# Optimization experiments

Hardware: AMD Instinct MI355X
Metric: run time of the kernel (lower is better)

The kernel has to match this reference:

```python
import jax, jax.numpy as jnp
import numpy as np

N = 10000   # nodes
E = 320000  # edges
B = 4       # batch
D = 128     # in_dim == out_dim
H = 4       # heads
DH = D // H # 32, per-head dim
OUT_L = D // H  # per-layer out_fc output dim (out_dim/num_heads)
NEG_SLOPE = 0.1


def setup_inputs() -> dict:
    key = jax.random.key(0)
    ks = jax.random.split(key, 20)
    inp = {
        "features": jax.random.normal(ks[0], (B, N, D), dtype=jnp.float32),
        "src": jax.random.randint(ks[1], (E,), 0, N),
        "dst": jax.random.randint(ks[2], (E,), 0, N),
        "edge_w": jax.random.uniform(ks[3], (E,), dtype=jnp.float32),
    }
    s = 0.05
    for l in range(2):
        k = 4 + 5 * l
        inp[f"fc_w{l}"] = jax.random.normal(ks[k], (D, D), dtype=jnp.float32) * s
        inp[f"al{l}"] = jax.random.normal(ks[k + 1], (H, DH), dtype=jnp.float32) * s
        inp[f"ar{l}"] = jax.random.normal(ks[k + 2], (H, DH), dtype=jnp.float32) * s
        inp[f"out_w{l}"] = jax.random.normal(ks[k + 3], (OUT_L, DH), dtype=jnp.float32) * s
        inp[f"out_b{l}"] = jnp.zeros((OUT_L,), dtype=jnp.float32)
    inp["mlp_w"] = jax.random.normal(ks[14], (D, 2 * D), dtype=jnp.float32) * s
    inp["mlp_b"] = jnp.zeros((D,), dtype=jnp.float32)
    return inp


def _gat_layer(x, src, dst, w, fc_w, al, ar, out_w, out_b):
    # x: [B,N,D]
    feat = jnp.einsum("bnd,ed->bne", x, fc_w).reshape(B, N, H, DH)  # fc, no bias
    el = jnp.einsum("bnhd,hd->bnh", feat, al)  # [B,N,H]
    er = jnp.einsum("bnhd,hd->bnh", feat, ar)
    # per-edge scores, edge-major: [E,B,H]
    e = jnp.moveaxis(el[:, src] + er[:, dst], 1, 0)
    e = jnp.where(e > 0, e, NEG_SLOPE * e)        # LeakyReLU(0.1)
    e = e * w[:, None, None]                      # edge weight applied pre-softmax
    # edge-softmax over incoming edges of each dst node
    m = jax.ops.segment_max(e, dst, num_segments=N)
    m = jnp.where(jnp.isfinite(m), m, 0.0)
    ex = jnp.exp(e - m[dst])
    den = jax.ops.segment_sum(ex, dst, num_segments=N)[dst]
    a = ex / jnp.where(den == 0, 1.0, den)        # [E,B,H]
    # u_mul_e + sum aggregation
    feat_n = jnp.moveaxis(feat, 0, 1)             # [N,B,H,DH]
    msg = feat_n[src] * a[..., None]              # [E,B,H,DH]
    agg = jax.ops.segment_sum(msg, dst, num_segments=N)  # [N,B,H,DH]
    out = jax.nn.relu(jnp.einsum("nbhd,od->nbho", agg, out_w) + out_b)
    # transpose(0,1) then concat heads along feature dim -> [B,N,H*OUT_L]
    return jnp.moveaxis(out, 0, 1).reshape(B, N, H * OUT_L)


def reference(features, src, dst, edge_w,
              fc_w0, al0, ar0, out_w0, out_b0,
              fc_w1, al1, ar1, out_w1, out_b1,
              mlp_w, mlp_b):
    x1 = _gat_layer(features, src, dst, edge_w, fc_w0, al0, ar0, out_w0, out_b0)
    x2 = _gat_layer(x1, src, dst, edge_w, fc_w1, al1, ar1, out_w1, out_b1)
    h = jnp.concatenate([x1, x2], axis=-1)        # [B,N,2*D]
    return jnp.einsum("bnk,ok->bno", h, mlp_w) + mlp_b  # eval mode: dropout off
```

## Files before the change

kernel.cpp:

```cpp
#include <hip/hip_runtime.h>
#include <hip/hip_fp16.h>
#include <float.h>

#define NN 10000
#define EE 320000
#define BB 4
#define DD 128
#define HH 4
#define DHH 32

union H4 { uint2 u2; __half2 h2[2]; };
union H8 { float4 f4; __half2 h2[4]; };

typedef _Float16 f16x8 __attribute__((ext_vector_type(8)));
typedef float f32x4 __attribute__((ext_vector_type(4)));

__global__ void pack_weights(const float* __restrict__ fc0, const float* __restrict__ fc1,
                             const float* __restrict__ mlp,
                             __half* __restrict__ bp0, __half* __restrict__ bp1,
                             __half* __restrict__ bpm,
                             int* __restrict__ cnt, int* __restrict__ cursor) {
    int s = blockIdx.x * 256 + threadIdx.x;
    int i = s & 7, l = (s >> 3) & 63, ct = (s >> 9) & 7, kt = s >> 12;
    int k = kt * 32 + 8 * (l >> 4) + i;
    int o = ct * 16 + (l & 15);
    bpm[s] = __float2half(mlp[o * 256 + k]);
    if (s < 16384) {
        bp0[s] = __float2half(fc0[o * 128 + k]);
        bp1[s] = __float2half(fc1[o * 128 + k]);
    }
    if (s < NN) { cnt[s] = 0; cursor[s] = 0; }
}

__global__ void count_edges(const int* __restrict__ dst, int* __restrict__ cnt) {
    int e = blockIdx.x * 256 + threadIdx.x;
    if (e < EE) atomicAdd(&cnt[dst[e]], 1);
}

__global__ void scan_kernel(const int* __restrict__ cnt, int* __restrict__ row_off) {
    __shared__ int part[1024];
    int t = threadIdx.x;
    const int CH = 10;
    int loc[CH];
    int s = 0;
#pragma unroll
    for (int j = 0; j < CH; ++j) {
        int i = t * CH + j;
        int v = (i < NN) ? cnt[i] : 0;
        loc[j] = s;
        s += v;
    }
    part[t] = s;
    __syncthreads();
    for (int off = 1; off < 1024; off <<= 1) {
        int v = (t >= off) ? part[t - off] : 0;
        __syncthreads();
        part[t] += v;
        __syncthreads();
    }
    int pre = (t > 0) ? part[t - 1] : 0;
#pragma unroll
    for (int j = 0; j < CH; ++j) {
        int i = t * CH + j;
        if (i < NN) row_off[i] = pre + loc[j];
    }
    if (t == 0) row_off[NN] = part[1023];
}

__global__ void scatter_edges(const int* __restrict__ dst, const int* __restrict__ row_off,
                              int* __restrict__ cursor, int* __restrict__ edge_ids) {
    int e = blockIdx.x * 256 + threadIdx.x;
    if (e < EE) {
        int d = dst[e];
        int p = atomicAdd(&cursor[d], 1);
        edge_ids[row_off[d] + p] = e;
    }
}

template <int K, bool A_HALF, bool HALF_OUT, bool BIAS>
__global__ __launch_bounds__(256) void mfma_gemm(
    const void* __restrict__ A_, int lda,
    const __half* __restrict__ Bp,
    const float* __restrict__ bias,
    __half* __restrict__ outh, float* __restrict__ outf, int ldo) {
    __shared__ __half A_s[64 * K];
    int tid = threadIdx.x;
    int row0 = blockIdx.x * 64;

    if (A_HALF) {
        const __half* A = (const __half*)A_;
#pragma unroll
        for (int it = 0; it < (64 * K / 8) / 256; ++it) {
            int s = it * 256 + tid;
            int r = s / (K / 8), c8 = s % (K / 8);
            uint4 v = *reinterpret_cast<const uint4*>(A + (size_t)(row0 + r) * lda + c8 * 8);
            int byte = (r * K + c8 * 8) * 2;
            byte ^= (r & 7) << 4;
            *reinterpret_cast<uint4*>((char*)A_s + byte) = v;
        }
    } else {
        const float* A = (const float*)A_;
#pragma unroll
        for (int it = 0; it < (64 * K / 4) / 256; ++it) {
            int s = it * 256 + tid;
            int r = s / (K / 4), c4 = s % (K / 4);
            float4 v = *reinterpret_cast<const float4*>(A + (size_t)(row0 + r) * lda + c4 * 4);
            __half h[4];
            h[0] = __float2half(v.x); h[1] = __float2half(v.y);
            h[2] = __float2half(v.z); h[3] = __float2half(v.w);
            int byte = (r * K + c4 * 4) * 2;
            byte ^= (r & 7) << 4;
            *reinterpret_cast<uint2*>((char*)A_s + byte) = *reinterpret_cast<uint2*>(h);
        }
    }
    __syncthreads();

    int l = tid & 63, w = tid >> 6;
    int g = l >> 4, r15 = l & 15;
    f32x4 acc[8] = {};

#pragma unroll
    for (int kt = 0; kt < K / 32; ++kt) {
        int row = w * 16 + r15;
        int byte = (row * K + kt * 32 + 8 * g) * 2;
        byte ^= (row & 7) << 4;
        f16x8 a = *reinterpret_cast<const f16x8*>((const char*)A_s + byte);
        const f16x8* bp = reinterpret_cast<const f16x8*>(Bp) + (size_t)(kt * 8) * 64 + l;
#pragma unroll
        for (int ct = 0; ct < 8; ++ct) {
            f16x8 b = bp[(size_t)ct * 64];
            acc[ct] = __builtin_amdgcn_mfma_f32_16x16x32_f16(a, b, acc[ct], 0, 0, 0);
        }
    }

#pragma unroll
    for (int ct = 0; ct < 8; ++ct) {
        int col = ct * 16 + r15;
#pragma unroll
        for (int reg = 0; reg < 4; ++reg) {
            int row = row0 + w * 16 + g * 4 + reg;
            float v = acc[ct][reg];
            if (BIAS) v += bias[col];
            if (HALF_OUT) outh[(size_t)row * ldo + col] = __float2half(v);
            else outf[(size_t)row * ldo + col] = v;
        }
    }
}

__global__ __launch_bounds__(256) void elr_kernel(
    const __half* __restrict__ feat_h, const float* __restrict__ al,
    const float* __restrict__ ar, float* __restrict__ el, float* __restrict__ er) {
    __shared__ float s_al[128], s_ar[128];
    int tid = threadIdx.x;
    if (tid < 128) s_al[tid] = al[tid];
    else s_ar[tid - 128] = ar[tid - 128];
    __syncthreads();
    int idx = blockIdx.x * 256 + tid;
    if (idx < BB * NN * HH) {
        int h = idx & 3;
        const __half* row = feat_h + (size_t)(idx >> 2) * 128 + h * 32;
        float al_acc = 0.f, ar_acc = 0.f;
#pragma unroll
        for (int q = 0; q < 8; ++q) {
            H4 u;
            u.u2 = *reinterpret_cast<const uint2*>(row + q * 4);
            float2 f0 = __half22float2(u.h2[0]);
            float2 f1 = __half22float2(u.h2[1]);
            int d = h * 32 + q * 4;
            al_acc += f0.x * s_al[d] + f0.y * s_al[d + 1] + f1.x * s_al[d + 2] + f1.y * s_al[d + 3];
            ar_acc += f0.x * s_ar[d] + f0.y * s_ar[d + 1] + f1.x * s_ar[d + 2] + f1.y * s_ar[d + 3];
        }
        el[idx] = al_acc;
        er[idx] = ar_acc;
    }
}

#define PSTR 66
__global__ __launch_bounds__(256) void gat_aggregate(
    const int* __restrict__ row_off, const int* __restrict__ edge_ids,
    const int* __restrict__ src, const float* __restrict__ ew,
    const float* __restrict__ el, const float* __restrict__ er,
    const __half* __restrict__ feat_h, const float* __restrict__ out_w,
    const float* __restrict__ out_b, __half* __restrict__ hcat, int layer_off) {
    __shared__ float s_owt[32 * 33];
    __shared__ int s_srcA[4][64];
    __shared__ float s_wA[4][64];
    __shared__ float s_pA[4][16 * PSTR];

    int tid = threadIdx.x;
    for (int i = tid; i < 1024; i += 256) {
        int o = i >> 5, d = i & 31;
        s_owt[d * 33 + o] = out_w[i];
    }
    __syncthreads();

    int wv = tid >> 6, lane = tid & 63;
    int n = blockIdx.x * 4 + wv;
    int start = row_off[n], end = row_off[n + 1];
    int* s_src = s_srcA[wv];
    float* s_w = s_wA[wv];
    float* s_p = s_pA[wv];

    int bh = lane & 15, sl = lane >> 4;
    int b = bh >> 2, h = bh & 3;
    float er1 = er[((size_t)b * NN + n) * 4 + h];
    const __half* fbase = feat_h + (size_t)b * NN * 128 + h * 32 + sl * 8;

    float m_reg = -FLT_MAX, den_reg = 0.f;
    float acc8[8];
#pragma unroll
    for (int i = 0; i < 8; ++i) acc8[i] = 0.f;

    for (int base = start; base < end; base += 64) {
        int cnum = end - base;
        if (cnum > 64) cnum = 64;
        if (lane < cnum) {
            int eid = edge_ids[base + lane];
            s_src[lane] = src[eid];
            s_w[lane] = ew[eid];
        }
        float lmax = -FLT_MAX;
#pragma unroll 4
        for (int j = sl; j < cnum; j += 4) {
            int s = s_src[j];
            float sc = el[((size_t)b * NN + s) * 4 + h] + er1;
            sc = sc > 0.f ? sc : 0.1f * sc;
            sc *= s_w[j];
            s_p[bh * PSTR + j] = sc;
            lmax = fmaxf(lmax, sc);
        }
        lmax = fmaxf(lmax, __shfl_xor(lmax, 16, 64));
        lmax = fmaxf(lmax, __shfl_xor(lmax, 32, 64));
        float m_new = fmaxf(m_reg, lmax);
        float scale = __expf(m_reg - m_new);
        m_reg = m_new;
        float lden = 0.f;
#pragma unroll 4
        for (int j = sl; j < cnum; j += 4) {
            float p = __expf(s_p[bh * PSTR + j] - m_new);
            s_p[bh * PSTR + j] = p;
            lden += p;
        }
        lden += __shfl_xor(lden, 16, 64);
        lden += __shfl_xor(lden, 32, 64);
        den_reg = den_reg * scale + lden;
#pragma unroll
        for (int i = 0; i < 8; ++i) acc8[i] *= scale;
#pragma unroll 8
        for (int j = 0; j < cnum; ++j) {
            float p = s_p[bh * PSTR + j];
            int s = s_src[j];
            H8 u;
            u.f4 = *reinterpret_cast<const float4*>(fbase + (size_t)s * 128);
            float2 f0 = __half22float2(u.h2[0]);
            float2 f1 = __half22float2(u.h2[1]);
            float2 f2 = __half22float2(u.h2[2]);
            float2 f3 = __half22float2(u.h2[3]);
            acc8[0] += p * f0.x; acc8[1] += p * f0.y;
            acc8[2] += p * f1.x; acc8[3] += p * f1.y;
            acc8[4] += p * f2.x; acc8[5] += p * f2.y;
            acc8[6] += p * f3.x; acc8[7] += p * f3.y;
        }
    }

    float inv_den = (den_reg == 0.f) ? 1.f : 1.f / den_reg;
#pragma unroll
    for (int i = 0; i < 8; ++i) s_p[bh * PSTR + sl * 8 + i] = acc8[i] * inv_den;

    float o_acc[8];
#pragma unroll
    for (int i = 0; i < 8; ++i) o_acc[i] = out_b[sl * 8 + i];
#pragma unroll 8
    for (int dd = 0; dd < 32; ++dd) {
        float a = s_p[bh * PSTR + dd];
        const float* wr = s_owt + dd * 33 + sl * 8;
#pragma unroll
        for (int i = 0; i < 8; ++i) o_acc[i] += a * wr[i];
    }
    H8 ov;
#pragma unroll
    for (int k = 0; k < 4; ++k)
        ov.h2[k] = __floats2half2_rn(fmaxf(o_acc[2 * k], 0.f), fmaxf(o_acc[2 * k + 1], 0.f));
    *reinterpret_cast<float4*>(hcat + ((size_t)b * NN + n) * 256 + layer_off + h * 32 + sl * 8) = ov.f4;
}

extern "C" void kernel_launch(void* const* d_in, const int* in_sizes, int n_in,
                              void* d_out, int out_size, void* d_ws, size_t ws_size,
                              hipStream_t stream) {
    const float* features = (const float*)d_in[0];
    const int* src = (const int*)d_in[1];
    const int* dst = (const int*)d_in[2];
    const float* edge_w = (const float*)d_in[3];
    const float* fc_w0 = (const float*)d_in[4];
    const float* al0 = (const float*)d_in[5];
    const float* ar0 = (const float*)d_in[6];
    const float* out_w0 = (const float*)d_in[7];
    const float* out_b0 = (const float*)d_in[8];
    const float* fc_w1 = (const float*)d_in[9];
    const float* al1 = (const float*)d_in[10];
    const float* ar1 = (const float*)d_in[11];
    const float* out_w1 = (const float*)d_in[12];
    const float* out_b1 = (const float*)d_in[13];
    const float* mlp_w = (const float*)d_in[14];
    const float* mlp_b = (const float*)d_in[15];
    float* out = (float*)d_out;

    char* p = (char*)d_ws;
    auto take = [&](size_t bytes) {
        char* cur = p;
        p += (bytes + 255) & ~(size_t)255;
        return cur;
    };
    __half* bp0 = (__half*)take(16384 * 2);
    __half* bp1 = (__half*)take(16384 * 2);
    __half* bpm = (__half*)take(32768 * 2);
    __half* feat_h = (__half*)take((size_t)BB * NN * 128 * 2);
    __half* hcat = (__half*)take((size_t)BB * NN * 256 * 2);
    float* el = (float*)take((size_t)BB * NN * HH * 4);
    float* er = (float*)take((size_t)BB * NN * HH * 4);
    int* cnt = (int*)take((size_t)NN * 4);
    int* cursor = (int*)take((size_t)NN * 4);
    int* row_off = (int*)take((size_t)(NN + 1) * 4);
    int* edge_ids = (int*)take((size_t)EE * 4);
    (void)ws_size; (void)in_sizes; (void)n_in; (void)out_size;

    pack_weights<<<128, 256, 0, stream>>>(fc_w0, fc_w1, mlp_w, bp0, bp1, bpm, cnt, cursor);
    count_edges<<<EE / 256, 256, 0, stream>>>(dst, cnt);
    scan_kernel<<<1, 1024, 0, stream>>>(cnt, row_off);
    scatter_edges<<<EE / 256, 256, 0, stream>>>(dst, row_off, cursor, edge_ids);

    const int GEMM_GRID = (BB * NN) / 64;
    const int ELR_GRID = (BB * NN * HH + 255) / 256;
    const int AGG_GRID = NN / 4;

    mfma_gemm<128, false, true, false><<<GEMM_GRID, 256, 0, stream>>>(
        features, 128, bp0, nullptr, feat_h, nullptr, 128);
    elr_kernel<<<ELR_GRID, 256, 0, stream>>>(feat_h, al0, ar0, el, er);
    gat_aggregate<<<AGG_GRID, 256, 0, stream>>>(row_off, edge_ids, src, edge_w, el, er,
                                                feat_h, out_w0, out_b0, hcat, 0);
    mfma_gemm<128, true, true, false><<<GEMM_GRID, 256, 0, stream>>>(
        hcat, 256, bp1, nullptr, feat_h, nullptr, 128);
    elr_kernel<<<ELR_GRID, 256, 0, stream>>>(feat_h, al1, ar1, el, er);
    gat_aggregate<<<AGG_GRID, 256, 0, stream>>>(row_off, edge_ids, src, edge_w, el, er,
                                                feat_h, out_w1, out_b1, hcat, 128);
    mfma_gemm<256, true, false, true><<<GEMM_GRID, 256, 0, stream>>>(
        hcat, 256, bpm, mlp_b, nullptr, out, 128);
}
```

Baseline: 211.2 us.

## Split GAT aggregation per batch with wave-level edge parallelism and cross-lane reduction

The aggregate kernel now launches one block per (batch, node-group) instead of one wave handling all four batches of a node. Within a wave, lanes split the edge loop four ways, each covering a 128-wide feature slice, and partial sums are reduced with shuffles. The output projection is recomputed with two outputs per lane. Block ordering interleaves batches so nearby blocks share node indices, which is meant to improve L2 reuse of graph metadata while giving each batch's gathers a contiguous feature row. In exchange, edge metadata and scores are loaded four times (once per batch) and extra shuffle reductions are added.

```diff
diff --git a/kernel.cpp b/kernel.cpp
--- a/kernel.cpp
+++ b/kernel.cpp
@@ -175,7 +175,6 @@
     }
 }
 
-#define PSTR 66
 __global__ __launch_bounds__(256) void gat_aggregate(
     const int* __restrict__ row_off, const int* __restrict__ edge_ids,
     const int* __restrict__ src, const float* __restrict__ ew,
@@ -185,7 +184,8 @@
     __shared__ float s_owt[32 * 33];
     __shared__ int s_srcA[4][64];
     __shared__ float s_wA[4][64];
-    __shared__ float s_pA[4][16 * PSTR];
+    __shared__ float s_pA[4][256];
+    __shared__ float s_aggA[4][4 * 36];
 
     int tid = threadIdx.x;
     for (int i = tid; i < 1024; i += 256) {
@@ -194,17 +194,24 @@
     }
     __syncthreads();
 
+    int g = blockIdx.x;
+    int b = (g & 7) >> 1;
+    int ngrp = ((g >> 3) << 1) | (g & 1);
     int wv = tid >> 6, lane = tid & 63;
-    int n = blockIdx.x * 4 + wv;
+    int n = ngrp * 4 + wv;
     int start = row_off[n], end = row_off[n + 1];
+
     int* s_src = s_srcA[wv];
     float* s_w = s_wA[wv];
     float* s_p = s_pA[wv];
-
-    int bh = lane & 15, sl = lane >> 4;
-    int b = bh >> 2, h = bh & 3;
-    float er1 = er[((size_t)b * NN + n) * 4 + h];
-    const __half* fbase = feat_h + (size_t)b * NN * 128 + h * 32 + sl * 8;
+    float* s_agg = s_aggA[wv];
+
+    int h1 = lane >> 4, jslot = lane & 15;
+    int jj = lane >> 4, t = lane & 15;
+    int h2 = t >> 2;
+    const float* el_b = el + (size_t)b * NN * 4;
+    float er1 = er[((size_t)b * NN + n) * 4 + h1];
+    const __half* fbase = feat_h + (size_t)b * NN * 128 + t * 8;
 
     float m_reg = -FLT_MAX, den_reg = 0.f;
     float acc8[8];
@@ -221,34 +228,35 @@
         }
         float lmax = -FLT_MAX;
 #pragma unroll 4
-        for (int j = sl; j < cnum; j += 4) {
+        for (int j = jslot; j < cnum; j += 16) {
             int s = s_src[j];
-            float sc = el[((size_t)b * NN + s) * 4 + h] + er1;
+            float sc = el_b[s * 4 + h1] + er1;
             sc = sc > 0.f ? sc : 0.1f * sc;
             sc *= s_w[j];
-            s_p[bh * PSTR + j] = sc;
+            s_p[j * 4 + h1] = sc;
             lmax = fmaxf(lmax, sc);
         }
-        lmax = fmaxf(lmax, __shfl_xor(lmax, 16, 64));
-        lmax = fmaxf(lmax, __shfl_xor(lmax, 32, 64));
+#pragma unroll
+        for (int mk = 1; mk <= 8; mk <<= 1) lmax = fmaxf(lmax, __shfl_xor(lmax, mk, 64));
         float m_new = fmaxf(m_reg, lmax);
-        float scale = __expf(m_reg - m_new);
+        float scale1 = __expf(m_reg - m_new);
         m_reg = m_new;
         float lden = 0.f;
 #pragma unroll 4
-        for (int j = sl; j < cnum; j += 4) {
-            float p = __expf(s_p[bh * PSTR + j] - m_new);
-            s_p[bh * PSTR + j] = p;
-            lden += p;
-        }
-        lden += __shfl_xor(lden, 16, 64);
-        lden += __shfl_xor(lden, 32, 64);
-        den_reg = den_reg * scale + lden;
-#pragma unroll
-        for (int i = 0; i < 8; ++i) acc8[i] *= scale;
-#pragma unroll 8
-        for (int j = 0; j < cnum; ++j) {
-            float p = s_p[bh * PSTR + j];
+        for (int j = jslot; j < cnum; j += 16) {
+            float pv = __expf(s_p[j * 4 + h1] - m_new);
+            s_p[j * 4 + h1] = pv;
+            lden += pv;
+        }
+#pragma unroll
+        for (int mk = 1; mk <= 8; mk <<= 1) lden += __shfl_xor(lden, mk, 64);
+        den_reg = den_reg * scale1 + lden;
+        float scale2 = __shfl(scale1, h2 << 4, 64);
+#pragma unroll
+        for (int i = 0; i < 8; ++i) acc8[i] *= scale2;
+#pragma unroll 4
+        for (int j = jj; j < cnum; j += 4) {
+            float pv = s_p[j * 4 + h2];
             int s = s_src[j];
             H8 u;
             u.f4 = *reinterpret_cast<const float4*>(fbase + (size_t)s * 128);
@@ -256,32 +264,35 @@
             float2 f1 = __half22float2(u.h2[1]);
             float2 f2 = __half22float2(u.h2[2]);
             float2 f3 = __half22float2(u.h2[3]);
-            acc8[0] += p * f0.x; acc8[1] += p * f0.y;
-            acc8[2] += p * f1.x; acc8[3] += p * f1.y;
-            acc8[4] += p * f2.x; acc8[5] += p * f2.y;
-            acc8[6] += p * f3.x; acc8[7] += p * f3.y;
-        }
-    }
-
-    float inv_den = (den_reg == 0.f) ? 1.f : 1.f / den_reg;
-#pragma unroll
-    for (int i = 0; i < 8; ++i) s_p[bh * PSTR + sl * 8 + i] = acc8[i] * inv_den;
-
-    float o_acc[8];
-#pragma unroll
-    for (int i = 0; i < 8; ++i) o_acc[i] = out_b[sl * 8 + i];
+            acc8[0] += pv * f0.x; acc8[1] += pv * f0.y;
+            acc8[2] += pv * f1.x; acc8[3] += pv * f1.y;
+            acc8[4] += pv * f2.x; acc8[5] += pv * f2.y;
+            acc8[6] += pv * f3.x; acc8[7] += pv * f3.y;
+        }
+    }
+
+#pragma unroll
+    for (int i = 0; i < 8; ++i) {
+        acc8[i] += __shfl_xor(acc8[i], 16, 64);
+        acc8[i] += __shfl_xor(acc8[i], 32, 64);
+    }
+    float den = __shfl(den_reg, h2 << 4, 64);
+    float inv_den = (den == 0.f) ? 1.f : 1.f / den;
+    if (jj == 0) {
+        int sub = t & 3;
+#pragma unroll
+        for (int i = 0; i < 8; ++i) s_agg[h2 * 36 + sub * 8 + i] = acc8[i] * inv_den;
+    }
+    int h3 = lane >> 4, oo = (lane & 15) * 2;
+    float o0 = out_b[oo], o1 = out_b[oo + 1];
 #pragma unroll 8
-    for (int dd = 0; dd < 32; ++dd) {
-        float a = s_p[bh * PSTR + dd];
-        const float* wr = s_owt + dd * 33 + sl * 8;
-#pragma unroll
-        for (int i = 0; i < 8; ++i) o_acc[i] += a * wr[i];
-    }
-    H8 ov;
-#pragma unroll
-    for (int k = 0; k < 4; ++k)
-        ov.h2[k] = __floats2half2_rn(fmaxf(o_acc[2 * k], 0.f), fmaxf(o_acc[2 * k + 1], 0.f));
-    *reinterpret_cast<float4*>(hcat + ((size_t)b * NN + n) * 256 + layer_off + h * 32 + sl * 8) = ov.f4;
+    for (int d = 0; d < 32; ++d) {
+        float a = s_agg[h3 * 36 + d];
+        o0 += a * s_owt[d * 33 + oo];
+        o1 += a * s_owt[d * 33 + oo + 1];
+    }
+    __half2 hv = __floats2half2_rn(fmaxf(o0, 0.f), fmaxf(o1, 0.f));
+    *reinterpret_cast<__half2*>(hcat + ((size_t)b * NN + n) * 256 + layer_off + h3 * 32 + oo) = hv;
 }
 
 extern "C" void kernel_launch(void* const* d_in, const int* in_sizes, int n_in,
@@ -331,7 +342,7 @@
 
     const int GEMM_GRID = (BB * NN) / 64;
     const int ELR_GRID = (BB * NN * HH + 255) / 256;
-    const int AGG_GRID = NN / 4;
+    const int AGG_GRID = NN;
 
     mfma_gemm<128, false, true, false><<<GEMM_GRID, 256, 0, stream>>>(
         features, 128, bp0, nullptr, feat_h, nullptr, 128);
```

New measurement: 236.7 us. 1.12x slower.

## Fuse attention logit computation into fc GEMM epilogue and use 128-row tiles

Applied to the files above, without the earlier changes.

Removes the separate elr_kernel by computing el/er directly from the MFMA accumulators in the fc GEMM epilogue, using per-lane multiplies by al/ar and a 16-lane shuffle reduction. This avoids re-reading the fp16 features and one kernel launch per layer. The fc GEMMs also process 128 rows per block (two row tiles per wave), with clamped loads and guarded stores for the ragged tail. Attention logits now come from fp32 accumulators instead of fp16-rounded features, which changes numerics slightly, and the larger tiles reduce the block count.

```diff
diff --git a/kernel.cpp b/kernel.cpp
--- a/kernel.cpp
+++ b/kernel.cpp
@@ -77,23 +77,28 @@
     }
 }
 
-template <int K, bool A_HALF, bool HALF_OUT, bool BIAS>
+template <int K, int ROWS, bool A_HALF, bool ATTN, bool HALF_OUT, bool BIAS>
 __global__ __launch_bounds__(256) void mfma_gemm(
     const void* __restrict__ A_, int lda,
     const __half* __restrict__ Bp,
+    const float* __restrict__ al, const float* __restrict__ ar,
     const float* __restrict__ bias,
-    __half* __restrict__ outh, float* __restrict__ outf, int ldo) {
-    __shared__ __half A_s[64 * K];
+    __half* __restrict__ outh, float* __restrict__ outf, int ldo,
+    float* __restrict__ el_out, float* __restrict__ er_out) {
+    constexpr int RT = ROWS / 64;
+    __shared__ __half A_s[ROWS * K];
+    const int gmax = BB * NN;
     int tid = threadIdx.x;
-    int row0 = blockIdx.x * 64;
+    int row0 = blockIdx.x * ROWS;
 
     if (A_HALF) {
         const __half* A = (const __half*)A_;
 #pragma unroll
-        for (int it = 0; it < (64 * K / 8) / 256; ++it) {
+        for (int it = 0; it < (ROWS * K / 8) / 256; ++it) {
             int s = it * 256 + tid;
             int r = s / (K / 8), c8 = s % (K / 8);
-            uint4 v = *reinterpret_cast<const uint4*>(A + (size_t)(row0 + r) * lda + c8 * 8);
+            int gr = row0 + r; if (gr >= gmax) gr = gmax - 1;
+            uint4 v = *reinterpret_cast<const uint4*>(A + (size_t)gr * lda + c8 * 8);
             int byte = (r * K + c8 * 8) * 2;
             byte ^= (r & 7) << 4;
             *reinterpret_cast<uint4*>((char*)A_s + byte) = v;
@@ -101,10 +106,11 @@
     } else {
         const float* A = (const float*)A_;
 #pragma unroll
-        for (int it = 0; it < (64 * K / 4) / 256; ++it) {
+        for (int it = 0; it < (ROWS * K / 4) / 256; ++it) {
             int s = it * 256 + tid;
             int r = s / (K / 4), c4 = s % (K / 4);
-            float4 v = *reinterpret_cast<const float4*>(A + (size_t)(row0 + r) * lda + c4 * 4);
+            int gr = row0 + r; if (gr >= gmax) gr = gmax - 1;
+            float4 v = *reinterpret_cast<const float4*>(A + (size_t)gr * lda + c4 * 4);
             __half h[4];
             h[0] = __float2half(v.x); h[1] = __float2half(v.y);
             h[2] = __float2half(v.z); h[3] = __float2half(v.w);
@@ -117,61 +123,76 @@
 
     int l = tid & 63, w = tid >> 6;
     int g = l >> 4, r15 = l & 15;
-    f32x4 acc[8] = {};
+    f32x4 acc[RT][8] = {};
 
 #pragma unroll
     for (int kt = 0; kt < K / 32; ++kt) {
-        int row = w * 16 + r15;
-        int byte = (row * K + kt * 32 + 8 * g) * 2;
-        byte ^= (row & 7) << 4;
-        f16x8 a = *reinterpret_cast<const f16x8*>((const char*)A_s + byte);
         const f16x8* bp = reinterpret_cast<const f16x8*>(Bp) + (size_t)(kt * 8) * 64 + l;
 #pragma unroll
+        for (int rt = 0; rt < RT; ++rt) {
+            int row = w * (16 * RT) + rt * 16 + r15;
+            int byte = (row * K + kt * 32 + 8 * g) * 2;
+            byte ^= (row & 7) << 4;
+            f16x8 a = *reinterpret_cast<const f16x8*>((const char*)A_s + byte);
+#pragma unroll
+            for (int ct = 0; ct < 8; ++ct) {
+                f16x8 b = bp[(size_t)ct * 64];
+                acc[rt][ct] = __builtin_amdgcn_mfma_f32_16x16x32_f16(a, b, acc[rt][ct], 0, 0, 0);
+            }
+        }
+    }
+
+#pragma unroll
+    for (int rt = 0; rt < RT; ++rt) {
+#pragma unroll
         for (int ct = 0; ct < 8; ++ct) {
-            f16x8 b = bp[(size_t)ct * 64];
-            acc[ct] = __builtin_amdgcn_mfma_f32_16x16x32_f16(a, b, acc[ct], 0, 0, 0);
-        }
-    }
-
-#pragma unroll
-    for (int ct = 0; ct < 8; ++ct) {
-        int col = ct * 16 + r15;
-#pragma unroll
-        for (int reg = 0; reg < 4; ++reg) {
-            int row = row0 + w * 16 + g * 4 + reg;
-            float v = acc[ct][reg];
-            if (BIAS) v += bias[col];
-            if (HALF_OUT) outh[(size_t)row * ldo + col] = __float2half(v);
-            else outf[(size_t)row * ldo + col] = v;
-        }
-    }
-}
-
-__global__ __launch_bounds__(256) void elr_kernel(
-    const __half* __restrict__ feat_h, const float* __restrict__ al,
-    const float* __restrict__ ar, float* __restrict__ el, float* __restrict__ er) {
-    __shared__ float s_al[128], s_ar[128];
-    int tid = threadIdx.x;
-    if (tid < 128) s_al[tid] = al[tid];
-    else s_ar[tid - 128] = ar[tid - 128];
-    __syncthreads();
-    int idx = blockIdx.x * 256 + tid;
-    if (idx < BB * NN * HH) {
-        int h = idx & 3;
-        const __half* row = feat_h + (size_t)(idx >> 2) * 128 + h * 32;
-        float al_acc = 0.f, ar_acc = 0.f;
-#pragma unroll
-        for (int q = 0; q < 8; ++q) {
-            H4 u;
-            u.u2 = *reinterpret_cast<const uint2*>(row + q * 4);
-            float2 f0 = __half22float2(u.h2[0]);
-            float2 f1 = __half22float2(u.h2[1]);
-            int d = h * 32 + q * 4;
-            al_acc += f0.x * s_al[d] + f0.y * s_al[d + 1] + f1.x * s_al[d + 2] + f1.y * s_al[d + 3];
-            ar_acc += f0.x * s_ar[d] + f0.y * s_ar[d + 1] + f1.x * s_ar[d + 2] + f1.y * s_ar[d + 3];
-        }
-        el[idx] = al_acc;
-        er[idx] = ar_acc;
+            int col = ct * 16 + r15;
+#pragma unroll
+            for (int reg = 0; reg < 4; ++reg) {
+                int row = row0 + w * (16 * RT) + rt * 16 + g * 4 + reg;
+                if (row < gmax) {
+                    float v = acc[rt][ct][reg];
+                    if (BIAS) v += bias[col];
+                    if (HALF_OUT) outh[(size_t)row * ldo + col] = __float2half(v);
+                    else outf[(size_t)row * ldo + col] = v;
+                }
+            }
+        }
+    }
+
+    if (ATTN) {
+#pragma unroll
+        for (int rt = 0; rt < RT; ++rt) {
+#pragma unroll
+            for (int h = 0; h < 4; ++h) {
+                float al0 = al[(2 * h) * 16 + r15], al1 = al[(2 * h + 1) * 16 + r15];
+                float ar0 = ar[(2 * h) * 16 + r15], ar1 = ar[(2 * h + 1) * 16 + r15];
+                f32x4 pe, pr;
+#pragma unroll
+                for (int reg = 0; reg < 4; ++reg) {
+                    pe[reg] = acc[rt][2 * h][reg] * al0 + acc[rt][2 * h + 1][reg] * al1;
+                    pr[reg] = acc[rt][2 * h][reg] * ar0 + acc[rt][2 * h + 1][reg] * ar1;
+                }
+#pragma unroll
+                for (int mk = 1; mk <= 8; mk <<= 1) {
+#pragma unroll
+                    for (int reg = 0; reg < 4; ++reg) {
+                        pe[reg] += __shfl_xor(pe[reg], mk, 64);
+                        pr[reg] += __shfl_xor(pr[reg], mk, 64);
+                    }
+                }
+                if (r15 == 0) {
+#pragma unroll
+                    for (int reg = 0; reg < 4; ++reg) {
+                        int row = row0 + w * (16 * RT) + rt * 16 + g * 4 + reg;
+                        if (row < gmax) {
+                            el_out[row * 4 + h] = pe[reg];
+                            er_out[row * 4 + h] = pr[reg];
+                        }
+                    }
+                }
+            }
+        }
     }
 }
 
@@ -329,20 +350,18 @@
     scan_kernel<<<1, 1024, 0, stream>>>(cnt, row_off);
     scatter_edges<<<EE / 256, 256, 0, stream>>>(dst, row_off, cursor, edge_ids);
 
-    const int GEMM_GRID = (BB * NN) / 64;
-    const int ELR_GRID = (BB * NN * HH + 255) / 256;
+    const int GEMM_GRID = (BB * NN + 127) / 128;
+    const int MLP_GRID = (BB * NN) / 64;
     const int AGG_GRID = NN / 4;
 
-    mfma_gemm<128, false, true, false><<<GEMM_GRID, 256, 0, stream>>>(
-        features, 128, bp0, nullptr, feat_h, nullptr, 128);
-    elr_kernel<<<ELR_GRID, 256, 0, stream>>>(feat_h, al0, ar0, el, er);
+    mfma_gemm<128, 128, false, true, true, false><<<GEMM_GRID, 256, 0, stream>>>(
+        features, 128, bp0, al0, ar0, nullptr, feat_h, nullptr, 128, el, er);
     gat_aggregate<<<AGG_GRID, 256, 0, stream>>>(row_off, edge_ids, src, edge_w, el, er,
                                                 feat_h, out_w0, out_b0, hcat, 0);
-    mfma_gemm<128, true, true, false><<<GEMM_GRID, 256, 0, stream>>>(
-        hcat, 256, bp1, nullptr, feat_h, nullptr, 128);
-    elr_kernel<<<ELR_GRID, 256, 0, stream>>>(feat_h, al1, ar1, el, er);
+    mfma_gemm<128, 128, true, true, true, false><<<GEMM_GRID, 256, 0, stream>>>(
+        hcat, 256, bp1, al1, ar1, nullptr, feat_h, nullptr, 128, el, er);
     gat_aggregate<<<AGG_GRID, 256, 0, stream>>>(row_off, edge_ids, src, edge_w, el, er,
                                                 feat_h, out_w1, out_b1, hcat, 128);
-    mfma_gemm<256, true, false, true><<<GEMM_GRID, 256, 0, stream>>>(
-        hcat, 256, bpm, mlp_b, nullptr, out, 128);
-}
+    mfma_gemm<256, 64, true, false, false, true><<<MLP_GRID, 256, 0, stream>>>(
+        hcat, 256, bpm, nullptr, nullptr, mlp_b, nullptr, out, 128, nullptr, nullptr);
+}
```

Result: slower. 221.7 us (+5.0%).
